# Optimization experiments

Hardware: AMD Instinct MI355X
Metric: run time of the kernel (lower is better)

## Reference

```python
import jax, jax.numpy as jnp
import numpy as np

B, T, N, K = 16, 12, 2048, 20


def setup_inputs() -> dict:
    key = jax.random.key(0)
    k1, k2, k3, k4 = jax.random.split(key, 4)
    x = jax.random.normal(k1, (B, T, N, 1), dtype=jnp.float32)
    A_physical = jax.random.uniform(k2, (N, N), dtype=jnp.float32)
    W = jax.random.normal(k3, (16, 1), dtype=jnp.float32) / jnp.sqrt(1.0)
    b = jax.random.normal(k4, (16,), dtype=jnp.float32) * 0.01
    alpha = jnp.zeros((), dtype=jnp.float32)  # sigmoid(0) = 0.5
    return {"x": x, "A_physical": A_physical, "W": W, "b": b, "alpha": alpha}


def reference(x, A_physical, W, b, alpha):
    Bsz, Tlen, n, _ = x.shape
    # mean over time -> node state [B, N, 1]
    state = x.mean(axis=1)
    # fc_start + tanh -> [B, N, 16]
    state_emb = jnp.tanh(jnp.einsum("bni,hi->bnh", state, W) + b)
    # pairwise similarity [B, N, N]
    A_dyn = jnp.einsum("bnh,bmh->bnm", state_emb, state_emb)
    A_dyn = jax.nn.relu(A_dyn)
    k = min(K, n)
    topk_vals, topk_idx = jax.lax.top_k(A_dyn, k)  # [B, N, k]
    # scatter top-k values into a -inf mask, then row softmax
    neg_inf = jnp.full_like(A_dyn, -jnp.inf)
    b_idx = jnp.arange(Bsz)[:, None, None]
    n_idx = jnp.arange(n)[None, :, None]
    sparse = neg_inf.at[b_idx, n_idx, topk_idx].set(topk_vals)
    A_dyn_sm = jax.nn.softmax(sparse, axis=2)
    # row-normalized physical graph, broadcast over batch
    A_phys = A_physical / (A_physical.sum(axis=-1, keepdims=True) + 1e-8)
    a = jax.nn.sigmoid(alpha)
    A_final = a * A_phys[None, :, :] + (1.0 - a) * A_dyn_sm
    return A_final
```

## Files before the change

kernel.cpp:

```cpp
#include <hip/hip_runtime.h>
#include <math.h>

#define NB 16
#define NT 12
#define NN 2048
#define NH 16
#define NK 20

#define RPWV 16
#define CCAP 64

static __device__ __forceinline__ unsigned long long shflxor64(unsigned long long v, int m) {
  unsigned lo = (unsigned)v, hi = (unsigned)(v >> 32);
  lo = (unsigned)__shfl_xor((int)lo, m, 64);
  hi = (unsigned)__shfl_xor((int)hi, m, 64);
  return ((unsigned long long)hi << 32) | lo;
}

static __device__ __forceinline__ float dotQ(const float* q, const float4& e0,
                                             const float4& e1, const float4& e2,
                                             const float4& e3) {
  float a = 0.0f;
  a = __fmaf_rn(q[0], e0.x, a);  a = __fmaf_rn(q[1], e0.y, a);
  a = __fmaf_rn(q[2], e0.z, a);  a = __fmaf_rn(q[3], e0.w, a);
  a = __fmaf_rn(q[4], e1.x, a);  a = __fmaf_rn(q[5], e1.y, a);
  a = __fmaf_rn(q[6], e1.z, a);  a = __fmaf_rn(q[7], e1.w, a);
  a = __fmaf_rn(q[8], e2.x, a);  a = __fmaf_rn(q[9], e2.y, a);
  a = __fmaf_rn(q[10], e2.z, a); a = __fmaf_rn(q[11], e2.w, a);
  a = __fmaf_rn(q[12], e3.x, a); a = __fmaf_rn(q[13], e3.y, a);
  a = __fmaf_rn(q[14], e3.z, a); a = __fmaf_rn(q[15], e3.w, a);
  return a;
}

__global__ void k_emb(const float* __restrict__ x, const float* __restrict__ W,
                      const float* __restrict__ bias, float* __restrict__ emb) {
  int id = blockIdx.x * blockDim.x + threadIdx.x;
  if (id >= NB * NN) return;
  int b = id >> 11, n = id & (NN - 1);
  const float* xp = x + ((size_t)b * NT) * NN + n;
  float s = 0.0f;
#pragma unroll
  for (int t = 0; t < NT; ++t) s += xp[(size_t)t * NN];
  s = s / 12.0f;
  float* e = emb + (size_t)id * NH;
#pragma unroll
  for (int h = 0; h < NH; ++h) {
    float arg = __fadd_rn(__fmul_rn(s, W[h]), bias[h]);
    e[h] = (float)tanh((double)arg);
  }
}

__global__ void k_rowsum(const float* __restrict__ A, const float* __restrict__ alpha,
                         float* __restrict__ aInv) {
  int gw = (blockIdx.x * blockDim.x + threadIdx.x) >> 6;
  int lane = threadIdx.x & 63;
  if (gw >= NN) return;
  const float* row = A + (size_t)gw * NN;
  float s = 0.0f;
#pragma unroll
  for (int j = 0; j < NN / 64; ++j) s += row[lane + 64 * j];
#pragma unroll
  for (int off = 32; off; off >>= 1) s += __shfl_xor(s, off, 64);
  if (lane == 0) {
    float a = 1.0f / (1.0f + expf(-alpha[0]));
    aInv[gw] = a / (s + 1e-8f);
  }
}

__global__ __launch_bounds__(256) void k_topk(
    const float* __restrict__ emb, const float* __restrict__ Ap,
    const float* __restrict__ aInv, const float* __restrict__ alpha,
    unsigned short* __restrict__ fixIdx, float* __restrict__ fixVal) {
  __shared__ unsigned short candIdx[4][RPWV][CCAP];
  __shared__ int candCnt[4][RPWV];
  __shared__ float thL[4][RPWV];
  __shared__ unsigned long long fsel[4][NK];

  const int lane = threadIdx.x & 63;
  const int wv = threadIdx.x >> 6;
  const int gw = blockIdx.x * 4 + wv;
  const int b = gw >> 7;
  const int rbase = (gw & 127) * RPWV;
  const float* embB = emb + (size_t)b * NN * NH;

  if (lane < RPWV) candCnt[wv][lane] = 0;

  float rmax[RPWV];
#pragma unroll
  for (int r = 0; r < RPWV; ++r) rmax[r] = -1.0f;

#pragma unroll 1
  for (int et = 0; et < 8; ++et) {
    asm volatile("" ::: "memory");
    const float* p0 = embB + (size_t)(et * 256 + lane) * NH;
    float4 a0 = *(const float4*)(p0 + 0), a1 = *(const float4*)(p0 + 4),
           a2 = *(const float4*)(p0 + 8), a3 = *(const float4*)(p0 + 12);
    const float* p1 = p0 + 64 * NH;
    float4 b0 = *(const float4*)(p1 + 0), b1 = *(const float4*)(p1 + 4),
           b2 = *(const float4*)(p1 + 8), b3 = *(const float4*)(p1 + 12);
    const float* p2 = p1 + 64 * NH;
    float4 c0 = *(const float4*)(p2 + 0), c1 = *(const float4*)(p2 + 4),
           c2 = *(const float4*)(p2 + 8), c3 = *(const float4*)(p2 + 12);
    const float* p3 = p2 + 64 * NH;
    float4 d0 = *(const float4*)(p3 + 0), d1 = *(const float4*)(p3 + 4),
           d2 = *(const float4*)(p3 + 8), d3 = *(const float4*)(p3 + 12);
#pragma unroll
    for (int r = 0; r < RPWV; ++r) {
      const float* qp = embB + (size_t)(rbase + r) * NH;
      float qv[16];
#pragma unroll
      for (int h = 0; h < 16; ++h) qv[h] = qp[h];
      float v0 = fmaxf(dotQ(qv, a0, a1, a2, a3), 0.0f);
      float v1 = fmaxf(dotQ(qv, b0, b1, b2, b3), 0.0f);
      float v2 = fmaxf(dotQ(qv, c0, c1, c2, c3), 0.0f);
      float v3 = fmaxf(dotQ(qv, d0, d1, d2, d3), 0.0f);
      rmax[r] = fmaxf(rmax[r], fmaxf(fmaxf(v0, v1), fmaxf(v2, v3)));
    }
  }

#pragma unroll 1
  for (int r = 0; r < RPWV; ++r) {
    float v = rmax[r];
#pragma unroll
    for (int k = 2; k <= 64; k <<= 1) {
#pragma unroll
      for (int m = k >> 1; m > 0; m >>= 1) {
        float o = __shfl_xor(v, m, 64);
        bool up = (lane & k) != 0;
        bool takeMax = ((lane & m) == 0) ^ up;
        v = takeMax ? fmaxf(v, o) : fminf(v, o);
      }
    }
    float t19 = __shfl(v, 19, 64);
    if (lane == 0) thL[wv][r] = t19;
  }
  asm volatile("s_waitcnt lgkmcnt(0)" ::: "memory");

#pragma unroll 1
  for (int et = 0; et < 8; ++et) {
    asm volatile("" ::: "memory");
    const float* p0 = embB + (size_t)(et * 256 + lane) * NH;
    float4 a0 = *(const float4*)(p0 + 0), a1 = *(const float4*)(p0 + 4),
           a2 = *(const float4*)(p0 + 8), a3 = *(const float4*)(p0 + 12);
    const float* p1 = p0 + 64 * NH;
    float4 b0 = *(const float4*)(p1 + 0), b1 = *(const float4*)(p1 + 4),
           b2 = *(const float4*)(p1 + 8), b3 = *(const float4*)(p1 + 12);
    const float* p2 = p1 + 64 * NH;
    float4 c0 = *(const float4*)(p2 + 0), c1 = *(const float4*)(p2 + 4),
           c2 = *(const float4*)(p2 + 8), c3 = *(const float4*)(p2 + 12);
    const float* p3 = p2 + 64 * NH;
    float4 d0 = *(const float4*)(p3 + 0), d1 = *(const float4*)(p3 + 4),
           d2 = *(const float4*)(p3 + 8), d3 = *(const float4*)(p3 + 12);
#pragma unroll
    for (int r = 0; r < RPWV; ++r) {
      const float* qp = embB + (size_t)(rbase + r) * NH;
      float qv[16];
#pragma unroll
      for (int h = 0; h < 16; ++h) qv[h] = qp[h];
      float v0 = fmaxf(dotQ(qv, a0, a1, a2, a3), 0.0f);
      float v1 = fmaxf(dotQ(qv, b0, b1, b2, b3), 0.0f);
      float v2 = fmaxf(dotQ(qv, c0, c1, c2, c3), 0.0f);
      float v3 = fmaxf(dotQ(qv, d0, d1, d2, d3), 0.0f);
      float t = thL[wv][r];
      if (v0 >= t) { int s = atomicAdd(&candCnt[wv][r], 1); if (s < CCAP) candIdx[wv][r][s] = (unsigned short)(et * 256 + lane); }
      if (v1 >= t) { int s = atomicAdd(&candCnt[wv][r], 1); if (s < CCAP) candIdx[wv][r][s] = (unsigned short)(et * 256 + 64 + lane); }
      if (v2 >= t) { int s = atomicAdd(&candCnt[wv][r], 1); if (s < CCAP) candIdx[wv][r][s] = (unsigned short)(et * 256 + 128 + lane); }
      if (v3 >= t) { int s = atomicAdd(&candCnt[wv][r], 1); if (s < CCAP) candIdx[wv][r][s] = (unsigned short)(et * 256 + 192 + lane); }
    }
  }
  asm volatile("s_waitcnt lgkmcnt(0)" ::: "memory");

  float a_sig = 1.0f / (1.0f + expf(-alpha[0]));
  float oma = 1.0f - a_sig;

#pragma unroll 1
  for (int r = 0; r < RPWV; ++r) {
    const int row = rbase + r;
    const float* qp = embB + (size_t)row * NH;
    float qv[16];
#pragma unroll
    for (int h = 0; h < 16; ++h) qv[h] = qp[h];

    int cnt = __builtin_amdgcn_readfirstlane(candCnt[wv][r]);
    unsigned long long key = 0ull;
    if (cnt <= CCAP) {
      if (lane < cnt) {
        unsigned ci = candIdx[wv][r][lane];
        const float* ep = embB + (size_t)ci * NH;
        float4 e0 = *(const float4*)(ep + 0), e1 = *(const float4*)(ep + 4),
               e2 = *(const float4*)(ep + 8), e3 = *(const float4*)(ep + 12);
        float dd = fmaxf(dotQ(qv, e0, e1, e2, e3), 0.0f);
        key = ((unsigned long long)__float_as_uint(dd) << 32) | (unsigned)(~ci);
      }
#pragma unroll
      for (int k = 2; k <= 64; k <<= 1) {
#pragma unroll
        for (int m = k >> 1; m > 0; m >>= 1) {
          unsigned long long o = shflxor64(key, m);
          bool up = (lane & k) != 0;
          bool takeMax = ((lane & m) == 0) ^ up;
          key = (takeMax == (key > o)) ? key : o;
        }
      }
    } else {
      unsigned taken = 0u;
#pragma unroll 1
      for (int sel = 0; sel < NK; ++sel) {
        float bv = -1.0f;
        int bs = 0;
#pragma unroll 1
        for (int s = 0; s < 32; ++s) {
          const float* ep = embB + (size_t)(s * 64 + lane) * NH;
          float4 e0 = *(const float4*)(ep + 0), e1 = *(const float4*)(ep + 4),
                 e2 = *(const float4*)(ep + 8), e3 = *(const float4*)(ep + 12);
          float dd = fmaxf(dotQ(qv, e0, e1, e2, e3), 0.0f);
          bool ok = ((taken >> s) & 1u) == 0u;
          bool bet = ok && (dd > bv);
          bv = bet ? dd : bv;
          bs = bet ? s : bs;
        }
        unsigned idx = (unsigned)(bs * 64 + lane);
        unsigned long long kk = ((unsigned long long)__float_as_uint(bv) << 32) | (unsigned)(~idx);
#pragma unroll
        for (int off = 32; off; off >>= 1) {
          unsigned long long o = shflxor64(kk, off);
          kk = (o > kk) ? o : kk;
        }
        unsigned wi = ~(unsigned)kk;
        if ((wi & 63u) == (unsigned)lane) taken |= (1u << (wi >> 6));
        if (lane == 0) fsel[wv][sel] = kk;
      }
      asm volatile("s_waitcnt lgkmcnt(0)" ::: "memory");
      key = (lane < NK) ? fsel[wv][lane] : 0ull;
    }

    int kl = (cnt < NK) ? cnt : NK;
    float vs = __uint_as_float((unsigned)(key >> 32));
    float vmax = __shfl(vs, 0, 64);
    float ex = (lane < kl) ? expf(vs - vmax) : 0.0f;
    float ssum = ex;
#pragma unroll
    for (int off = 32; off; off >>= 1) ssum += __shfl_xor(ssum, off, 64);
    if (lane < kl) {
      float w = ex / ssum;
      unsigned mi = ~(unsigned)key;
      float p = Ap[(size_t)row * NN + mi];
      size_t o20 = ((size_t)b * NN + row) * NK + lane;
      fixVal[o20] = __fadd_rn(__fmul_rn(p, aInv[row]), __fmul_rn(oma, w));
      fixIdx[o20] = (unsigned short)mi;
    }
  }
}

__global__ __launch_bounds__(256, 6) void k_out(
    const float* __restrict__ Ap, const float* __restrict__ aInv,
    const unsigned short* __restrict__ fixIdx, const float* __restrict__ fixVal,
    float* __restrict__ out) {
  const int tid = threadIdx.x;
  const int lane = tid & 63;
  const int q = tid >> 6;
  const int n = blockIdx.x;

  float ai = aInv[n];
  const float4* pr = (const float4*)(Ap + (size_t)n * NN);
  float4 o[8];
#pragma unroll
  for (int f = 0; f < 8; ++f) {
    float4 p = pr[lane + 64 * f];
    o[f].x = __fmul_rn(p.x, ai);
    o[f].y = __fmul_rn(p.y, ai);
    o[f].z = __fmul_rn(p.z, ai);
    o[f].w = __fmul_rn(p.w, ai);
  }

  unsigned short ii[4];
  float vv[4];
#pragma unroll
  for (int i = 0; i < 4; ++i) {
    int bb = q * 4 + i;
    if (lane < NK) {
      size_t o20 = ((size_t)bb * NN + n) * NK + lane;
      ii[i] = fixIdx[o20];
      vv[i] = fixVal[o20];
    }
  }

#pragma unroll
  for (int i = 0; i < 4; ++i) {
    int bb = q * 4 + i;
    float4* orow = (float4*)(out + ((size_t)bb * NN + n) * NN);
#pragma unroll
    for (int f = 0; f < 8; ++f) orow[lane + 64 * f] = o[f];
  }
  asm volatile("s_waitcnt vmcnt(0)" ::: "memory");
#pragma unroll
  for (int i = 0; i < 4; ++i) {
    if (lane < NK) {
      int bb = q * 4 + i;
      out[((size_t)bb * NN + n) * NN + (unsigned)ii[i]] = vv[i];
    }
  }
}

extern "C" void kernel_launch(void* const* d_in, const int* in_sizes, int n_in,
                              void* d_out, int out_size, void* d_ws, size_t ws_size,
                              hipStream_t stream) {
  const float* x = (const float*)d_in[0];
  const float* Ap = (const float*)d_in[1];
  const float* W = (const float*)d_in[2];
  const float* bb = (const float*)d_in[3];
  const float* alpha = (const float*)d_in[4];
  float* out = (float*)d_out;

  float* emb = (float*)d_ws;
  float* aInv = emb + (size_t)NB * NN * NH;
  float* fixVal = aInv + NN;
  unsigned short* fixIdx = (unsigned short*)(fixVal + (size_t)NB * NN * NK);

  hipLaunchKernelGGL(k_emb, dim3((NB * NN + 255) / 256), dim3(256), 0, stream,
                     x, W, bb, emb);
  hipLaunchKernelGGL(k_rowsum, dim3((NN * 64) / 256), dim3(256), 0, stream,
                     Ap, alpha, aInv);
  hipLaunchKernelGGL(k_topk, dim3(NB * NN / (4 * RPWV)), dim3(256), 0, stream,
                     emb, Ap, aInv, alpha, fixIdx, fixVal);
  hipLaunchKernelGGL(k_out, dim3(NN), dim3(256), 0, stream,
                     Ap, aInv, fixIdx, fixVal, out);
}
```

Baseline: 222.5 us.

## Shrink rows per wave and hold query embeddings in scalar registers

Rows handled per wavefront drop from 16 to 4, and the row/batch mapping is adjusted, so the top-k kernel launches four times as many waves to fill the GPU. Query embeddings are loaded once as float4 and made wave-uniform with readfirstlane. This replaces the per-iteration reload of the query rows. The threshold is kept in registers instead of LDS. In exchange, each embedding tile is re-read by four times as many waves. Indexing qs[r] inside the non-unrolled final loop may push the array into scratch memory.

Measured after the change: 236.2 us. 1.06x slower.

```diff
diff --git a/kernel.cpp b/kernel.cpp
--- a/kernel.cpp
+++ b/kernel.cpp
@@ -7,7 +7,7 @@
 #define NH 16
 #define NK 20
 
-#define RPWV 16
+#define RPWV 4
 #define CCAP 64
 
 static __device__ __forceinline__ unsigned long long shflxor64(unsigned long long v, int m) {
@@ -15,6 +15,10 @@
   lo = (unsigned)__shfl_xor((int)lo, m, 64);
   hi = (unsigned)__shfl_xor((int)hi, m, 64);
   return ((unsigned long long)hi << 32) | lo;
+}
+
+static __device__ __forceinline__ float rfl(float v) {
+  return __int_as_float(__builtin_amdgcn_readfirstlane(__float_as_int(v)));
 }
 
 static __device__ __forceinline__ float dotQ(const float* q, const float4& e0,
@@ -73,17 +77,29 @@
     unsigned short* __restrict__ fixIdx, float* __restrict__ fixVal) {
   __shared__ unsigned short candIdx[4][RPWV][CCAP];
   __shared__ int candCnt[4][RPWV];
-  __shared__ float thL[4][RPWV];
   __shared__ unsigned long long fsel[4][NK];
 
   const int lane = threadIdx.x & 63;
   const int wv = threadIdx.x >> 6;
   const int gw = blockIdx.x * 4 + wv;
-  const int b = gw >> 7;
-  const int rbase = (gw & 127) * RPWV;
+  const int b = gw >> 9;
+  const int rbase = (gw & 511) * RPWV;
   const float* embB = emb + (size_t)b * NN * NH;
 
   if (lane < RPWV) candCnt[wv][lane] = 0;
+  asm volatile("s_waitcnt lgkmcnt(0)" ::: "memory");
+
+  float qs[RPWV][NH];
+#pragma unroll
+  for (int r = 0; r < RPWV; ++r) {
+    const float* qp = embB + (size_t)(rbase + r) * NH;
+    float4 t0 = *(const float4*)(qp + 0),  t1 = *(const float4*)(qp + 4),
+           t2 = *(const float4*)(qp + 8),  t3 = *(const float4*)(qp + 12);
+    qs[r][0] = rfl(t0.x);  qs[r][1] = rfl(t0.y);  qs[r][2] = rfl(t0.z);  qs[r][3] = rfl(t0.w);
+    qs[r][4] = rfl(t1.x);  qs[r][5] = rfl(t1.y);  qs[r][6] = rfl(t1.z);  qs[r][7] = rfl(t1.w);
+    qs[r][8] = rfl(t2.x);  qs[r][9] = rfl(t2.y);  qs[r][10] = rfl(t2.z); qs[r][11] = rfl(t2.w);
+    qs[r][12] = rfl(t3.x); qs[r][13] = rfl(t3.y); qs[r][14] = rfl(t3.z); qs[r][15] = rfl(t3.w);
+  }
 
   float rmax[RPWV];
 #pragma unroll
@@ -91,34 +107,21 @@
 
 #pragma unroll 1
   for (int et = 0; et < 8; ++et) {
-    asm volatile("" ::: "memory");
-    const float* p0 = embB + (size_t)(et * 256 + lane) * NH;
-    float4 a0 = *(const float4*)(p0 + 0), a1 = *(const float4*)(p0 + 4),
-           a2 = *(const float4*)(p0 + 8), a3 = *(const float4*)(p0 + 12);
-    const float* p1 = p0 + 64 * NH;
-    float4 b0 = *(const float4*)(p1 + 0), b1 = *(const float4*)(p1 + 4),
-           b2 = *(const float4*)(p1 + 8), b3 = *(const float4*)(p1 + 12);
-    const float* p2 = p1 + 64 * NH;
-    float4 c0 = *(const float4*)(p2 + 0), c1 = *(const float4*)(p2 + 4),
-           c2 = *(const float4*)(p2 + 8), c3 = *(const float4*)(p2 + 12);
-    const float* p3 = p2 + 64 * NH;
-    float4 d0 = *(const float4*)(p3 + 0), d1 = *(const float4*)(p3 + 4),
-           d2 = *(const float4*)(p3 + 8), d3 = *(const float4*)(p3 + 12);
-#pragma unroll
-    for (int r = 0; r < RPWV; ++r) {
-      const float* qp = embB + (size_t)(rbase + r) * NH;
-      float qv[16];
-#pragma unroll
-      for (int h = 0; h < 16; ++h) qv[h] = qp[h];
-      float v0 = fmaxf(dotQ(qv, a0, a1, a2, a3), 0.0f);
-      float v1 = fmaxf(dotQ(qv, b0, b1, b2, b3), 0.0f);
-      float v2 = fmaxf(dotQ(qv, c0, c1, c2, c3), 0.0f);
-      float v3 = fmaxf(dotQ(qv, d0, d1, d2, d3), 0.0f);
-      rmax[r] = fmaxf(rmax[r], fmaxf(fmaxf(v0, v1), fmaxf(v2, v3)));
-    }
-  }
-
-#pragma unroll 1
+#pragma unroll 2
+    for (int j = 0; j < 4; ++j) {
+      const float* ep = embB + (size_t)(et * 256 + j * 64 + lane) * NH;
+      float4 e0 = *(const float4*)(ep + 0), e1 = *(const float4*)(ep + 4),
+             e2 = *(const float4*)(ep + 8), e3 = *(const float4*)(ep + 12);
+#pragma unroll
+      for (int r = 0; r < RPWV; ++r) {
+        float d = fmaxf(dotQ(qs[r], e0, e1, e2, e3), 0.0f);
+        rmax[r] = fmaxf(rmax[r], d);
+      }
+    }
+  }
+
+  float th[RPWV];
+#pragma unroll
   for (int r = 0; r < RPWV; ++r) {
     float v = rmax[r];
 #pragma unroll
@@ -131,41 +134,25 @@
         v = takeMax ? fmaxf(v, o) : fminf(v, o);
       }
     }
-    float t19 = __shfl(v, 19, 64);
-    if (lane == 0) thL[wv][r] = t19;
-  }
-  asm volatile("s_waitcnt lgkmcnt(0)" ::: "memory");
+    th[r] = rfl(__shfl(v, 19, 64));
+  }
 
 #pragma unroll 1
   for (int et = 0; et < 8; ++et) {
-    asm volatile("" ::: "memory");
-    const float* p0 = embB + (size_t)(et * 256 + lane) * NH;
-    float4 a0 = *(const float4*)(p0 + 0), a1 = *(const float4*)(p0 + 4),
-           a2 = *(const float4*)(p0 + 8), a3 = *(const float4*)(p0 + 12);
-    const float* p1 = p0 + 64 * NH;
-    float4 b0 = *(const float4*)(p1 + 0), b1 = *(const float4*)(p1 + 4),
-           b2 = *(const float4*)(p1 + 8), b3 = *(const float4*)(p1 + 12);
-    const float* p2 = p1 + 64 * NH;
-    float4 c0 = *(const float4*)(p2 + 0), c1 = *(const float4*)(p2 + 4),
-           c2 = *(const float4*)(p2 + 8), c3 = *(const float4*)(p2 + 12);
-    const float* p3 = p2 + 64 * NH;
-    float4 d0 = *(const float4*)(p3 + 0), d1 = *(const float4*)(p3 + 4),
-           d2 = *(const float4*)(p3 + 8), d3 = *(const float4*)(p3 + 12);
-#pragma unroll
-    for (int r = 0; r < RPWV; ++r) {
-      const float* qp = embB + (size_t)(rbase + r) * NH;
-      float qv[16];
-#pragma unroll
-      for (int h = 0; h < 16; ++h) qv[h] = qp[h];
-      float v0 = fmaxf(dotQ(qv, a0, a1, a2, a3), 0.0f);
-      float v1 = fmaxf(dotQ(qv, b0, b1, b2, b3), 0.0f);
-      float v2 = fmaxf(dotQ(qv, c0, c1, c2, c3), 0.0f);
-      float v3 = fmaxf(dotQ(qv, d0, d1, d2, d3), 0.0f);
-      float t = thL[wv][r];
-      if (v0 >= t) { int s = atomicAdd(&candCnt[wv][r], 1); if (s < CCAP) candIdx[wv][r][s] = (unsigned short)(et * 256 + lane); }
-      if (v1 >= t) { int s = atomicAdd(&candCnt[wv][r], 1); if (s < CCAP) candIdx[wv][r][s] = (unsigned short)(et * 256 + 64 + lane); }
-      if (v2 >= t) { int s = atomicAdd(&candCnt[wv][r], 1); if (s < CCAP) candIdx[wv][r][s] = (unsigned short)(et * 256 + 128 + lane); }
-      if (v3 >= t) { int s = atomicAdd(&candCnt[wv][r], 1); if (s < CCAP) candIdx[wv][r][s] = (unsigned short)(et * 256 + 192 + lane); }
+#pragma unroll 2
+    for (int j = 0; j < 4; ++j) {
+      const int node = et * 256 + j * 64 + lane;
+      const float* ep = embB + (size_t)node * NH;
+      float4 e0 = *(const float4*)(ep + 0), e1 = *(const float4*)(ep + 4),
+             e2 = *(const float4*)(ep + 8), e3 = *(const float4*)(ep + 12);
+#pragma unroll
+      for (int r = 0; r < RPWV; ++r) {
+        float d = fmaxf(dotQ(qs[r], e0, e1, e2, e3), 0.0f);
+        if (d >= th[r]) {
+          int s = atomicAdd(&candCnt[wv][r], 1);
+          if (s < CCAP) candIdx[wv][r][s] = (unsigned short)node;
+        }
+      }
     }
   }
   asm volatile("s_waitcnt lgkmcnt(0)" ::: "memory");
@@ -176,11 +163,6 @@
 #pragma unroll 1
   for (int r = 0; r < RPWV; ++r) {
     const int row = rbase + r;
-    const float* qp = embB + (size_t)row * NH;
-    float qv[16];
-#pragma unroll
-    for (int h = 0; h < 16; ++h) qv[h] = qp[h];
-
     int cnt = __builtin_amdgcn_readfirstlane(candCnt[wv][r]);
     unsigned long long key = 0ull;
     if (cnt <= CCAP) {
@@ -189,7 +171,7 @@
         const float* ep = embB + (size_t)ci * NH;
         float4 e0 = *(const float4*)(ep + 0), e1 = *(const float4*)(ep + 4),
                e2 = *(const float4*)(ep + 8), e3 = *(const float4*)(ep + 12);
-        float dd = fmaxf(dotQ(qv, e0, e1, e2, e3), 0.0f);
+        float dd = fmaxf(dotQ(qs[r], e0, e1, e2, e3), 0.0f);
         key = ((unsigned long long)__float_as_uint(dd) << 32) | (unsigned)(~ci);
       }
 #pragma unroll
@@ -213,7 +195,7 @@
           const float* ep = embB + (size_t)(s * 64 + lane) * NH;
           float4 e0 = *(const float4*)(ep + 0), e1 = *(const float4*)(ep + 4),
                  e2 = *(const float4*)(ep + 8), e3 = *(const float4*)(ep + 12);
-          float dd = fmaxf(dotQ(qv, e0, e1, e2, e3), 0.0f);
+          float dd = fmaxf(dotQ(qs[r], e0, e1, e2, e3), 0.0f);
           bool ok = ((taken >> s) & 1u) == 0u;
           bool bet = ok && (dd > bv);
           bv = bet ? dd : bv;
```
